# Kernel optimization log

Hardware: AMD Instinct MI355X
Metric: run time of the kernel (lower is better)

## Reference

```python
import jax, jax.numpy as jnp
import numpy as np

H, D_MODEL, LEN_Q, LEN_K, D_K, D_V = 16, 1024, 2048, 2048, 64, 64
BATCH = 4
SCALE = 1.0 / np.sqrt(float(D_K))


def setup_inputs() -> dict:
    key = jax.random.key(0)
    ks = jax.random.split(key, 10)
    inp = {
        "Q": jax.random.normal(ks[0], (BATCH, LEN_Q, D_MODEL), dtype=jnp.float32),
        "K": jax.random.normal(ks[1], (BATCH, LEN_K, D_MODEL), dtype=jnp.float32),
        "V": jax.random.normal(ks[2], (BATCH, LEN_K, D_MODEL), dtype=jnp.float32),
        "mask": jax.random.randint(ks[3], (BATCH, LEN_K), 0, 2, dtype=jnp.int32),
        # Linear params (torch Linear: y = x @ W.T + b); store W as [in, out].
        "Wq": jax.random.normal(ks[4], (D_MODEL, H * D_K), dtype=jnp.float32) * (1.0 / np.sqrt(D_MODEL)),
        "bq": jnp.zeros((H * D_K,), dtype=jnp.float32),
        "Wk": jax.random.normal(ks[5], (D_MODEL, H * D_K), dtype=jnp.float32) * (1.0 / np.sqrt(D_MODEL)),
        "bk": jnp.zeros((H * D_K,), dtype=jnp.float32),
        "Wv": jax.random.normal(ks[6], (D_MODEL, H * D_V), dtype=jnp.float32) * (1.0 / np.sqrt(D_MODEL)),
        "bv": jnp.zeros((H * D_V,), dtype=jnp.float32),
    }
    return inp


def reference(Q, K, V, mask, Wq, bq, Wk, bk, Wv, bv):
    B = Q.shape[0]
    # Projections -> [B, S, H, d]
    q = (Q @ Wq + bq).reshape(B, LEN_Q, H, D_K)
    k = (K @ Wk + bk).reshape(B, LEN_K, H, D_K)
    v = (V @ Wv + bv).reshape(B, LEN_K, H, D_V)
    # Scores: [B, H, len_q, len_k]
    scores = jnp.einsum("bqhd,bkhd->bhqk", q, k) * SCALE
    # Key-padding mask broadcast over heads and queries
    scores = jnp.where(mask[:, None, None, :] == 0, jnp.float32(-1e9), scores)
    alpha = jax.nn.softmax(scores, axis=-1)
    out = jnp.einsum("bhqk,bkhd->bqhd", alpha, v)  # [B, len_q, H, d_v]
    return out.reshape(B, LEN_Q, H * D_V)
```

## Files before the change

### kernel.cpp

```cpp
#include <hip/hip_runtime.h>

#define NH 16
#define DM 1024
#define SQ 2048
#define BT 4

typedef __attribute__((ext_vector_type(8))) short bf16x8;
typedef __attribute__((ext_vector_type(4))) short sh4;
typedef __attribute__((ext_vector_type(4))) float f4;
typedef __attribute__((ext_vector_type(4))) float fv4;
typedef __attribute__((ext_vector_type(4))) unsigned uv4;
typedef unsigned short u16;

#define M2BIAS 23.083120654f
#define SCALE2 0.18033688f

__device__ __forceinline__ u16 f2bf(float f) {
    union { float f; unsigned u; } v; v.f = f;
    unsigned r = v.u + 0x7FFFu + ((v.u >> 16) & 1u);
    return (u16)(r >> 16);
}

__device__ __forceinline__ float fast_exp2(float x) {
#if __has_builtin(__builtin_amdgcn_exp2f)
    return __builtin_amdgcn_exp2f(x);
#else
    return exp2f(x);
#endif
}

__device__ __forceinline__ int prem(int s) {
    return (s & ~31) | ((s & 4) << 2) | ((s >> 1) & 12) | (s & 3);
}

#define GLD16(gp, lp) __builtin_amdgcn_global_load_lds( \
    (const __attribute__((address_space(1))) void*)(gp), \
    (__attribute__((address_space(3))) void*)(lp), 16, 0, 0)

__global__ __launch_bounds__(256) void cvt_wT3(const float* __restrict__ W0, const float* __restrict__ W1,
                                               const float* __restrict__ W2, u16* __restrict__ Wt) {
    __shared__ float t[64][65];
    const float* Wsrc = blockIdx.z == 0 ? W0 : (blockIdx.z == 1 ? W1 : W2);
    u16* dst = Wt + (size_t)blockIdx.z * DM * DM;
    int r0 = blockIdx.x * 64, c0 = blockIdx.y * 64;
    #pragma unroll
    for (int i = 0; i < 16; ++i) {
        int idx = i * 256 + threadIdx.x;
        int r = idx >> 6, c = idx & 63;
        t[r][c] = Wsrc[(size_t)(r0 + r) * DM + c0 + c];
    }
    __syncthreads();
    #pragma unroll
    for (int i = 0; i < 16; ++i) {
        int idx = i * 256 + threadIdx.x;
        int n = idx >> 6, k = idx & 63;
        dst[(size_t)(c0 + n) * DM + r0 + k] = f2bf(t[k][n]);
    }
}

__global__ __launch_bounds__(256) void mk_mbias(const int* __restrict__ mask, float* __restrict__ mb) {
    int i = blockIdx.x * 256 + threadIdx.x;
    mb[prem(i)] = mask[i] ? -M2BIAS : -__builtin_inff();
}

__global__ __launch_bounds__(256, 3) void gemm3(const float* __restrict__ Qf, const float* __restrict__ Kf,
                                                const float* __restrict__ Vf, const u16* __restrict__ Wt3,
                                                const float* __restrict__ bq, const float* __restrict__ bk,
                                                const float* __restrict__ bv, u16* __restrict__ out3) {
    __shared__ u16 As[128 * 64];
    __shared__ u16 Bs[2][128 * 64];
    int z = blockIdx.z;
    const float* Af = z == 0 ? Qf : (z == 1 ? Kf : Vf);
    const float* bias = z == 0 ? bq : (z == 1 ? bk : bv);
    int vmode = z == 0 ? 0 : (z == 1 ? 2 : 1);
    const u16* Bg = Wt3 + (size_t)z * DM * DM + (size_t)blockIdx.y * 128 * DM;
    u16* outp = out3 + (size_t)z * 8388608u;

    int tid = threadIdx.x;
    int w = tid >> 6, lane = tid & 63, quad = lane >> 4, l16 = lane & 15;
    int wm = w >> 1, wn = w & 1;
    int r8 = lane >> 3, cg = (lane & 7) ^ r8;

    int arow0 = w * 32 + (lane >> 4);
    int acol = (lane & 15) * 4;
    const float* Ag = Af + (size_t)(blockIdx.x * 128 + arow0) * DM + acol;
    int ach = (lane & 15) >> 1, asub = lane & 1;

    f4 acc[4][4];
    #pragma unroll
    for (int mt = 0; mt < 4; ++mt)
        #pragma unroll
        for (int nt = 0; nt < 4; ++nt) acc[mt][nt] = f4{0.f, 0.f, 0.f, 0.f};

    fv4 ar[8];
    auto loadA = [&](int kt) {
        const float* src = Ag + kt * 64;
        #pragma unroll
        for (int j = 0; j < 8; ++j) ar[j] = *(const fv4*)(src + (size_t)j * 4 * DM);
    };
    auto stageB = [&](int buf, int kt) {
        int kofs = kt * 64 + cg * 8;
        #pragma unroll
        for (int c = 0; c < 4; ++c) {
            int rbase = w * 32 + c * 8;
            GLD16(Bg + (size_t)(rbase + r8) * DM + kofs, &Bs[buf][rbase * 64]);
        }
    };

    stageB(0, 0);
    loadA(0);

    for (int kt = 0; kt < 16; ++kt) {
        if (kt + 1 < 16) stageB((kt + 1) & 1, kt + 1);
        #pragma unroll
        for (int j = 0; j < 8; ++j) {
            unsigned lo, hi;
            asm("v_cvt_pk_bf16_f32 %0, %1, %2" : "=v"(lo) : "v"(ar[j][0]), "v"(ar[j][1]));
            asm("v_cvt_pk_bf16_f32 %0, %1, %2" : "=v"(hi) : "v"(ar[j][2]), "v"(ar[j][3]));
            int row = arow0 + j * 4;
            uint2 pk; pk.x = lo; pk.y = hi;
            *(uint2*)&As[row * 64 + (ach ^ (row & 7)) * 8 + asub * 4] = pk;
        }
        if (kt + 1 < 16) loadA(kt + 1);

        if (kt < 15) {
            asm volatile("s_waitcnt vmcnt(12) lgkmcnt(0)" ::: "memory");
        } else {
            asm volatile("s_waitcnt vmcnt(0) lgkmcnt(0)" ::: "memory");
        }
        __builtin_amdgcn_s_barrier();
        asm volatile("" ::: "memory");

        #pragma unroll
        for (int ks = 0; ks < 2; ++ks) {
            bf16x8 afr[4], bfr[4];
            #pragma unroll
            for (int mt = 0; mt < 4; ++mt) {
                int row = wm * 64 + mt * 16 + l16;
                int ch = (ks * 4 + quad) ^ (row & 7);
                afr[mt] = *(const bf16x8*)&As[row * 64 + ch * 8];
            }
            #pragma unroll
            for (int nt = 0; nt < 4; ++nt) {
                int row = wn * 64 + nt * 16 + l16;
                int ch = (ks * 4 + quad) ^ (row & 7);
                bfr[nt] = *(const bf16x8*)&Bs[kt & 1][row * 64 + ch * 8];
            }
            #pragma unroll
            for (int mt = 0; mt < 4; ++mt)
                #pragma unroll
                for (int nt = 0; nt < 4; ++nt)
                    acc[mt][nt] = __builtin_amdgcn_mfma_f32_16x16x32_bf16(afr[mt], bfr[nt], acc[mt][nt], 0, 0, 0);
        }
        asm volatile("" ::: "memory");
        __builtin_amdgcn_s_barrier();
        asm volatile("" ::: "memory");
    }

    #pragma unroll
    for (int nt = 0; nt < 4; ++nt) {
        int ncol = blockIdx.y * 128 + wn * 64 + nt * 16 + l16;
        float bn = bias[ncol];
        int h = ncol >> 6, d = ncol & 63;
        #pragma unroll
        for (int mt = 0; mt < 4; ++mt) {
            int mbase = blockIdx.x * 128 + wm * 64 + mt * 16 + quad * 4;
            int bidx = mbase >> 11, s0 = mbase & 2047;
            if (vmode == 1) {
                sh4 pk;
                #pragma unroll
                for (int reg = 0; reg < 4; ++reg) pk[reg] = (short)f2bf(acc[mt][nt][reg] + bn);
                *(sh4*)&outp[(((size_t)bidx * NH + h) * 64 + d) * SQ + s0] = pk;
            } else {
                int sp = (vmode == 2) ? prem(s0) : s0;
                size_t base = ((size_t)bidx * NH + h) * SQ;
                #pragma unroll
                for (int reg = 0; reg < 4; ++reg)
                    outp[(base + sp + reg) * 64 + d] = f2bf(acc[mt][nt][reg] + bn);
            }
        }
    }
}

__global__ __launch_bounds__(256, 4) void attn(const u16* __restrict__ qw, const u16* __restrict__ kw,
                                               const u16* __restrict__ vtw, const float* __restrict__ mbias,
                                               float* __restrict__ outp) {
    __shared__ u16 Ks[2][64 * 64];
    __shared__ u16 Vs[2][64 * 64];
    int tid = threadIdx.x;
    int w = tid >> 6, lane = tid & 63, quad = lane >> 4, l16 = lane & 15;
    int r8 = lane >> 3, sl = lane & 7;
    int bh = blockIdx.x, b = bh >> 4;
    int h = bh & 15;
    int qbase = blockIdx.y * 128 + w * 32;
    const u16* qp = qw + (size_t)bh * SQ * 64;
    const u16* kp = kw + (size_t)bh * SQ * 64;
    const u16* vp = vtw + (size_t)bh * 64 * SQ;
    const float* mbp = mbias + b * SQ;

    bf16x8 aq[2][2];
    #pragma unroll
    for (int mt = 0; mt < 2; ++mt)
        #pragma unroll
        for (int ks = 0; ks < 2; ++ks)
            aq[mt][ks] = *(const bf16x8*)&qp[(size_t)(qbase + mt * 16 + l16) * 64 + ks * 32 + quad * 8];

    f4 o[2][4];
    float lrow[2] = {0.f, 0.f};
    #pragma unroll
    for (int mt = 0; mt < 2; ++mt)
        #pragma unroll
        for (int nt = 0; nt < 4; ++nt) o[mt][nt] = f4{0.f, 0.f, 0.f, 0.f};

    auto stage = [&](int buf, int k0) {
        #pragma unroll
        for (int j = 0; j < 2; ++j) {
            int row = w * 16 + j * 8 + r8;
            int gsl = sl ^ (row & 7);
            GLD16(kp + (size_t)(k0 + row) * 64 + gsl * 8, &Ks[buf][(w * 16 + j * 8) * 64]);
            GLD16(vp + (size_t)row * SQ + k0 + gsl * 8, &Vs[buf][(w * 16 + j * 8) * 64]);
        }
    };

    stage(0, 0);
    for (int kb = 0; kb < 32; ++kb) {
        int buf = kb & 1;
        int k0 = kb * 64;
        __syncthreads();
        fv4 bias4[4];
        #pragma unroll
        for (int kt = 0; kt < 4; ++kt)
            bias4[kt] = *(const fv4*)&mbp[k0 + kt * 16 + quad * 4];
        if (kb + 1 < 32) stage(buf ^ 1, k0 + 64);

        bf16x8 bk[4][2];
        #pragma unroll
        for (int kt = 0; kt < 4; ++kt)
            #pragma unroll
            for (int ks = 0; ks < 2; ++ks) {
                int r = kt * 16 + l16;
                int slot = (ks * 4 + quad) ^ (r & 7);
                bk[kt][ks] = *(const bf16x8*)&Ks[buf][r * 64 + slot * 8];
            }
        f4 S[4][2];
        #pragma unroll
        for (int kt = 0; kt < 4; ++kt)
            #pragma unroll
            for (int mt = 0; mt < 2; ++mt) {
                f4 s = f4{0.f, 0.f, 0.f, 0.f};
                s = __builtin_amdgcn_mfma_f32_16x16x32_bf16(bk[kt][0], aq[mt][0], s, 0, 0, 0);
                s = __builtin_amdgcn_mfma_f32_16x16x32_bf16(bk[kt][1], aq[mt][1], s, 0, 0, 0);
                S[kt][mt] = s;
            }
        bf16x8 pa8[2][2];
        #pragma unroll
        for (int g = 0; g < 2; ++g)
            #pragma unroll
            for (int mt = 0; mt < 2; ++mt) {
                f4 se = S[2 * g][mt], so = S[2 * g + 1][mt];
                float p0 = fast_exp2(se[0] * SCALE2 + bias4[2 * g][0]);
                float p1 = fast_exp2(se[1] * SCALE2 + bias4[2 * g][1]);
                float p2 = fast_exp2(se[2] * SCALE2 + bias4[2 * g][2]);
                float p3 = fast_exp2(se[3] * SCALE2 + bias4[2 * g][3]);
                float q0 = fast_exp2(so[0] * SCALE2 + bias4[2 * g + 1][0]);
                float q1 = fast_exp2(so[1] * SCALE2 + bias4[2 * g + 1][1]);
                float q2 = fast_exp2(so[2] * SCALE2 + bias4[2 * g + 1][2]);
                float q3 = fast_exp2(so[3] * SCALE2 + bias4[2 * g + 1][3]);
                lrow[mt] += ((p0 + p1) + (p2 + p3)) + ((q0 + q1) + (q2 + q3));
                uv4 wv;
                wv[0] = (__float_as_uint(p1) & 0xFFFF0000u) | (__float_as_uint(p0) >> 16);
                wv[1] = (__float_as_uint(p3) & 0xFFFF0000u) | (__float_as_uint(p2) >> 16);
                wv[2] = (__float_as_uint(q1) & 0xFFFF0000u) | (__float_as_uint(q0) >> 16);
                wv[3] = (__float_as_uint(q3) & 0xFFFF0000u) | (__float_as_uint(q2) >> 16);
                pa8[g][mt] = __builtin_bit_cast(bf16x8, wv);
            }
        #pragma unroll
        for (int g = 0; g < 2; ++g) {
            bf16x8 bv8[4];
            #pragma unroll
            for (int nt = 0; nt < 4; ++nt) {
                int row = nt * 16 + l16;
                int ch = (g * 4 + quad) ^ (row & 7);
                bv8[nt] = *(const bf16x8*)&Vs[buf][row * 64 + ch * 8];
            }
            #pragma unroll
            for (int mt = 0; mt < 2; ++mt)
                #pragma unroll
                for (int nt = 0; nt < 4; ++nt)
                    o[mt][nt] = __builtin_amdgcn_mfma_f32_16x16x32_bf16(pa8[g][mt], bv8[nt], o[mt][nt], 0, 0, 0);
        }
    }

    #pragma unroll
    for (int mt = 0; mt < 2; ++mt) {
        float v = lrow[mt];
        v += __shfl_xor(v, 16);
        v += __shfl_xor(v, 32);
        #pragma unroll
        for (int reg = 0; reg < 4; ++reg) {
            float inv = 1.f / __shfl(v, quad * 4 + reg);
            int row = qbase + mt * 16 + quad * 4 + reg;
            size_t obase = ((size_t)b * SQ + row) * DM + h * 64;
            #pragma unroll
            for (int nt = 0; nt < 4; ++nt)
                outp[obase + nt * 16 + l16] = o[mt][nt][reg] * inv;
        }
    }
}

extern "C" void kernel_launch(void* const* d_in, const int* in_sizes, int n_in,
                              void* d_out, int out_size, void* d_ws, size_t ws_size,
                              hipStream_t stream) {
    (void)in_sizes; (void)n_in; (void)out_size; (void)ws_size;
    const float* Q  = (const float*)d_in[0];
    const float* K  = (const float*)d_in[1];
    const float* V  = (const float*)d_in[2];
    const int* mask = (const int*)d_in[3];
    const float* Wq = (const float*)d_in[4];
    const float* bq = (const float*)d_in[5];
    const float* Wk = (const float*)d_in[6];
    const float* bk = (const float*)d_in[7];
    const float* Wv = (const float*)d_in[8];
    const float* bv = (const float*)d_in[9];
    float* out = (float*)d_out;
    char* ws = (char*)d_ws;
    u16* q_ws  = (u16*)(ws);
    u16* k_ws  = (u16*)(ws + (size_t)16 * 1024 * 1024);
    u16* v_ws  = (u16*)(ws + (size_t)32 * 1024 * 1024);
    u16* wbuf3 = (u16*)(ws + (size_t)48 * 1024 * 1024);
    float* mb  = (float*)(ws + (size_t)54 * 1024 * 1024);

    cvt_wT3<<<dim3(16, 16, 3), 256, 0, stream>>>(Wq, Wk, Wv, wbuf3);
    mk_mbias<<<32, 256, 0, stream>>>(mask, mb);
    gemm3<<<dim3(64, 8, 3), 256, 0, stream>>>(Q, K, V, wbuf3, bq, bk, bv, q_ws);
    attn<<<dim3(64, 16), 256, 0, stream>>>(q_ws, k_ws, v_ws, mb, out);
}
```

Before: 319.7 us.

## Load GEMM A operand directly into MFMA fragments, bypassing LDS staging

The fp32 activation tile is no longer converted and written into a shared-memory A buffer. Each wave now loads its own rows from global memory in MFMA fragment layout, converts them to bf16 in registers, and overlaps the next half-k load with the current MFMAs. This removes the A LDS writes and reads and the LDS space they used. In exchange, the two waves sharing a row block both fetch the same A data from global memory, and the MFMAs can now wait on global load latency more directly.

```diff
diff --git a/kernel.cpp b/kernel.cpp
--- a/kernel.cpp
+++ b/kernel.cpp
@@ -67,7 +67,6 @@
                                                 const float* __restrict__ Vf, const u16* __restrict__ Wt3,
                                                 const float* __restrict__ bq, const float* __restrict__ bk,
                                                 const float* __restrict__ bv, u16* __restrict__ out3) {
-    __shared__ u16 As[128 * 64];
     __shared__ u16 Bs[2][128 * 64];
     int z = blockIdx.z;
     const float* Af = z == 0 ? Qf : (z == 1 ? Kf : Vf);
@@ -81,10 +80,7 @@
     int wm = w >> 1, wn = w & 1;
     int r8 = lane >> 3, cg = (lane & 7) ^ r8;
 
-    int arow0 = w * 32 + (lane >> 4);
-    int acol = (lane & 15) * 4;
-    const float* Ag = Af + (size_t)(blockIdx.x * 128 + arow0) * DM + acol;
-    int ach = (lane & 15) >> 1, asub = lane & 1;
+    const float* aF = Af + (size_t)(blockIdx.x * 128 + wm * 64 + l16) * DM + quad * 8;
 
     f4 acc[4][4];
     #pragma unroll
@@ -93,10 +89,25 @@
         for (int nt = 0; nt < 4; ++nt) acc[mt][nt] = f4{0.f, 0.f, 0.f, 0.f};
 
     fv4 ar[8];
-    auto loadA = [&](int kt) {
-        const float* src = Ag + kt * 64;
-        #pragma unroll
-        for (int j = 0; j < 8; ++j) ar[j] = *(const fv4*)(src + (size_t)j * 4 * DM);
+    auto loadA = [&](int kt, int ks) {
+        const float* s = aF + kt * 64 + ks * 32;
+        #pragma unroll
+        for (int mt = 0; mt < 4; ++mt) {
+            ar[2 * mt]     = *(const fv4*)(s + (size_t)mt * 16 * DM);
+            ar[2 * mt + 1] = *(const fv4*)(s + (size_t)mt * 16 * DM + 4);
+        }
+    };
+    auto cvtA = [&](bf16x8* pa) {
+        #pragma unroll
+        for (int mt = 0; mt < 4; ++mt) {
+            unsigned u0, u1, u2, u3;
+            asm("v_cvt_pk_bf16_f32 %0, %1, %2" : "=v"(u0) : "v"(ar[2 * mt][0]), "v"(ar[2 * mt][1]));
+            asm("v_cvt_pk_bf16_f32 %0, %1, %2" : "=v"(u1) : "v"(ar[2 * mt][2]), "v"(ar[2 * mt][3]));
+            asm("v_cvt_pk_bf16_f32 %0, %1, %2" : "=v"(u2) : "v"(ar[2 * mt + 1][0]), "v"(ar[2 * mt + 1][1]));
+            asm("v_cvt_pk_bf16_f32 %0, %1, %2" : "=v"(u3) : "v"(ar[2 * mt + 1][2]), "v"(ar[2 * mt + 1][3]));
+            uv4 wv; wv[0] = u0; wv[1] = u1; wv[2] = u2; wv[3] = u3;
+            pa[mt] = __builtin_bit_cast(bf16x8, wv);
+        }
     };
     auto stageB = [&](int buf, int kt) {
         int kofs = kt * 64 + cg * 8;
@@ -106,52 +117,40 @@
             GLD16(Bg + (size_t)(rbase + r8) * DM + kofs, &Bs[buf][rbase * 64]);
         }
     };
+    auto mfmaHalf = [&](int bufidx, int ks, const bf16x8* pa) {
+        bf16x8 bfr[4];
+        #pragma unroll
+        for (int nt = 0; nt < 4; ++nt) {
+            int row = wn * 64 + nt * 16 + l16;
+            int ch = (ks * 4 + quad) ^ (row & 7);
+            bfr[nt] = *(const bf16x8*)&Bs[bufidx][row * 64 + ch * 8];
+        }
+        #pragma unroll
+        for (int mt = 0; mt < 4; ++mt)
+            #pragma unroll
+            for (int nt = 0; nt < 4; ++nt)
+                acc[mt][nt] = __builtin_amdgcn_mfma_f32_16x16x32_bf16(pa[mt], bfr[nt], acc[mt][nt], 0, 0, 0);
+    };
 
     stageB(0, 0);
-    loadA(0);
+    loadA(0, 0);
 
     for (int kt = 0; kt < 16; ++kt) {
         if (kt + 1 < 16) stageB((kt + 1) & 1, kt + 1);
-        #pragma unroll
-        for (int j = 0; j < 8; ++j) {
-            unsigned lo, hi;
-            asm("v_cvt_pk_bf16_f32 %0, %1, %2" : "=v"(lo) : "v"(ar[j][0]), "v"(ar[j][1]));
-            asm("v_cvt_pk_bf16_f32 %0, %1, %2" : "=v"(hi) : "v"(ar[j][2]), "v"(ar[j][3]));
-            int row = arow0 + j * 4;
-            uint2 pk; pk.x = lo; pk.y = hi;
-            *(uint2*)&As[row * 64 + (ach ^ (row & 7)) * 8 + asub * 4] = pk;
-        }
-        if (kt + 1 < 16) loadA(kt + 1);
-
+        bf16x8 pa[4];
+        cvtA(pa);
+        loadA(kt, 1);
         if (kt < 15) {
-            asm volatile("s_waitcnt vmcnt(12) lgkmcnt(0)" ::: "memory");
+            asm volatile("s_waitcnt vmcnt(12)" ::: "memory");
         } else {
-            asm volatile("s_waitcnt vmcnt(0) lgkmcnt(0)" ::: "memory");
+            asm volatile("s_waitcnt vmcnt(8)" ::: "memory");
         }
         __builtin_amdgcn_s_barrier();
         asm volatile("" ::: "memory");
-
-        #pragma unroll
-        for (int ks = 0; ks < 2; ++ks) {
-            bf16x8 afr[4], bfr[4];
-            #pragma unroll
-            for (int mt = 0; mt < 4; ++mt) {
-                int row = wm * 64 + mt * 16 + l16;
-                int ch = (ks * 4 + quad) ^ (row & 7);
-                afr[mt] = *(const bf16x8*)&As[row * 64 + ch * 8];
-            }
-            #pragma unroll
-            for (int nt = 0; nt < 4; ++nt) {
-                int row = wn * 64 + nt * 16 + l16;
-                int ch = (ks * 4 + quad) ^ (row & 7);
-                bfr[nt] = *(const bf16x8*)&Bs[kt & 1][row * 64 + ch * 8];
-            }
-            #pragma unroll
-            for (int mt = 0; mt < 4; ++mt)
-                #pragma unroll
-                for (int nt = 0; nt < 4; ++nt)
-                    acc[mt][nt] = __builtin_amdgcn_mfma_f32_16x16x32_bf16(afr[mt], bfr[nt], acc[mt][nt], 0, 0, 0);
-        }
+        mfmaHalf(kt & 1, 0, pa);
+        cvtA(pa);
+        if (kt + 1 < 16) loadA(kt + 1, 0);
+        mfmaHalf(kt & 1, 1, pa);
         asm volatile("" ::: "memory");
         __builtin_amdgcn_s_barrier();
         asm volatile("" ::: "memory");
```

After: 409.3 us. 28.0% more time.
